# Kernel tuning notes

Measured on AMD Instinct MI355X. Metric: run time of the kernel, lower is better.

The kernel has to match this reference:

```python
import jax, jax.numpy as jnp
from jax import lax
import numpy as np

DIM = 256
QK = 256          # qk_dim defaults to dim
HEADS = 8
NWIN = 7
TOPK = 4
KS = 3            # side_dwconv


def setup_inputs() -> dict:
    key = jax.random.key(0)
    ks = jax.random.split(key, 8)
    B, H, W = 1, 112, 112
    s = lambda d: 1.0 / np.sqrt(d)
    return {
        "x": jax.random.normal(ks[0], (B, H, W, DIM), jnp.float32),
        # fused qkv linear: dim -> qk + qk + dim
        "w_qkv": jax.random.normal(ks[1], (DIM, 2 * QK + DIM), jnp.float32) * s(DIM),
        "b_qkv": jnp.zeros((2 * QK + DIM,), jnp.float32),
        # output projection
        "w_o": jax.random.normal(ks[2], (DIM, DIM), jnp.float32) * s(DIM),
        "b_o": jnp.zeros((DIM,), jnp.float32),
        # depthwise 3x3 lepe conv (HWIO with I=1, groups=dim)
        "lepe_w": jax.random.normal(ks[3], (KS, KS, 1, DIM), jnp.float32) * s(KS * KS),
        "lepe_b": jnp.zeros((DIM,), jnp.float32),
    }


def _win2img(t, B, H, W, c):
    # (B, p2, h, w, c) windows -> (B, H, W, c) image
    hw, ww = H // NWIN, W // NWIN
    t = t.reshape(B, NWIN, NWIN, hw, ww, c)
    return t.transpose(0, 1, 3, 2, 4, 5).reshape(B, H, W, c)


def reference(x, w_qkv, b_qkv, w_o, b_o, lepe_w, lepe_b):
    B, H, W, C = x.shape
    hw, ww = H // NWIN, W // NWIN
    p2, w2 = NWIN * NWIN, hw * ww
    hd_q, hd_v = QK // HEADS, DIM // HEADS
    scale = QK ** (-0.5)

    # partition into windows: (B, p2, hw, ww, C)
    xp = x.reshape(B, NWIN, hw, NWIN, ww, C).transpose(0, 1, 3, 2, 4, 5)
    xp = xp.reshape(B, p2, hw, ww, C)

    qkv = xp @ w_qkv + b_qkv
    q, kv = qkv[..., :QK], qkv[..., QK:]          # (B,p2,hw,ww,QK), (...,QK+DIM)

    q_pix = q.reshape(B, p2, w2, QK)
    kv_pix = kv.reshape(B, p2, w2, QK + DIM)      # identity kv_down

    # region-level routing (detached in original since diff_routing=False)
    q_win = lax.stop_gradient(q.mean((2, 3)))     # (B,p2,QK)
    k_win = lax.stop_gradient(kv[..., :QK].mean((2, 3)))
    logit = (q_win * scale) @ jnp.swapaxes(k_win, -1, -2)   # (B,p2,p2)
    top_logit, top_idx = lax.top_k(logit, TOPK)             # (B,p2,TOPK)
    r_weight = jax.nn.softmax(top_logit, axis=-1)           # unused: mul_weight='none'

    # gather top-k regions' KV: (B, p2, TOPK, w2, QK+DIM)
    kv_sel = jax.vmap(lambda kvb, idxb: kvb[idxb])(kv_pix, top_idx)

    k_sel = kv_sel[..., :QK].reshape(B, p2, TOPK * w2, HEADS, hd_q)
    v_sel = kv_sel[..., QK:].reshape(B, p2, TOPK * w2, HEADS, hd_v)
    qh = q_pix.reshape(B, p2, w2, HEADS, hd_q)

    attn = jnp.einsum('bpqhc,bpkhc->bphqk', qh * scale, k_sel)
    attn = jax.nn.softmax(attn, axis=-1)
    out = jnp.einsum('bphqk,bpkhc->bpqhc', attn, v_sel).reshape(B, p2, hw, ww, DIM)
    out = _win2img(out, B, H, W, DIM)

    # lepe: depthwise conv over v in image layout
    v_img = _win2img(kv[..., QK:], B, H, W, DIM)
    lepe = lax.conv_general_dilated(
        v_img, lepe_w, (1, 1), 'SAME',
        dimension_numbers=('NHWC', 'HWIO', 'NHWC'),
        feature_group_count=DIM) + lepe_b

    return (out + lepe) @ w_o + b_o
```

## Files before the change

### kernel.cpp

```cpp
#include <hip/hip_runtime.h>
#include <math.h>


typedef __bf16 bf16x8 __attribute__((ext_vector_type(8)));
typedef __bf16 bf16x4 __attribute__((ext_vector_type(4)));
typedef float f32x4 __attribute__((ext_vector_type(4)));

__global__ __launch_bounds__(64)
void pack1(const float* __restrict__ x, const float* __restrict__ w_qkv,
           const float* __restrict__ w_o, __bf16* __restrict__ xbf,
           __bf16* __restrict__ wtq, __bf16* __restrict__ wto) {
    const int b = blockIdx.x;
    const int t = threadIdx.x;
    if (b < 12544) {
        int p = b >> 8, pix = b & 255;
        int hh = (p / 7) * 16 + (pix >> 4);
        int ww = (p % 7) * 16 + (pix & 15);
        const float* src = x + ((size_t)(hh * 112 + ww)) * 256 + t * 4;
        float4 v = *(const float4*)src;
        bf16x4 o;
        o[0] = (__bf16)v.x; o[1] = (__bf16)v.y; o[2] = (__bf16)v.z; o[3] = (__bf16)v.w;
        *(bf16x4*)(xbf + (size_t)b * 256 + t * 4) = o;
    } else if (b < 12544 + 768) {
        int n = b - 12544;
        int k = t * 4;
        bf16x4 o;
        o[0] = (__bf16)w_qkv[(k + 0) * 768 + n];
        o[1] = (__bf16)w_qkv[(k + 1) * 768 + n];
        o[2] = (__bf16)w_qkv[(k + 2) * 768 + n];
        o[3] = (__bf16)w_qkv[(k + 3) * 768 + n];
        *(bf16x4*)(wtq + (size_t)n * 256 + k) = o;
    } else {
        int n = b - 12544 - 768;
        int k = t * 4;
        bf16x4 o;
        o[0] = (__bf16)w_o[(k + 0) * 256 + n];
        o[1] = (__bf16)w_o[(k + 1) * 256 + n];
        o[2] = (__bf16)w_o[(k + 2) * 256 + n];
        o[3] = (__bf16)w_o[(k + 3) * 256 + n];
        *(bf16x4*)(wto + (size_t)n * 256 + k) = o;
    }
}

template<int QKV>
__global__ __launch_bounds__(256)
void gemm_bf16(const __bf16* __restrict__ A,
               const __bf16* __restrict__ Wt,
               const float* __restrict__ bias,
               float* __restrict__ C, int N,
               __bf16* __restrict__ Qp,
               __bf16* __restrict__ Kp,
               __bf16* __restrict__ vbf,
               __bf16* __restrict__ Vt) {
    const int t = threadIdx.x & 63;
    const int wv = threadIdx.x >> 6;
    const int l16 = t & 15, quad = t >> 4;
    const int m0 = blockIdx.x * 64;
    const int n0 = blockIdx.y * 128 + wv * 32;

    __shared__ __bf16 Vs[128][72];

    f32x4 acc[2][4];
#pragma unroll
    for (int km = 0; km < 2; km++)
#pragma unroll
        for (int nt = 0; nt < 4; nt++) acc[km][nt] = (f32x4){0.f, 0.f, 0.f, 0.f};

#pragma unroll
    for (int ks = 0; ks < 8; ks++) {
        bf16x8 Af[2], Bf[4];
#pragma unroll
        for (int km = 0; km < 2; km++)
            Af[km] = *(const bf16x8*)(Wt + (size_t)(n0 + km * 16 + l16) * 256 + ks * 32 + quad * 8);
#pragma unroll
        for (int nt = 0; nt < 4; nt++)
            Bf[nt] = *(const bf16x8*)(A + (size_t)(m0 + nt * 16 + l16) * 256 + ks * 32 + quad * 8);
#pragma unroll
        for (int km = 0; km < 2; km++)
#pragma unroll
            for (int nt = 0; nt < 4; nt++)
                acc[km][nt] = __builtin_amdgcn_mfma_f32_16x16x32_bf16(
                    Af[km], Bf[nt], acc[km][nt], 0, 0, 0);
    }

#pragma unroll
    for (int km = 0; km < 2; km++) {
        const int n = n0 + km * 16 + quad * 4;
        float4 b4 = *(const float4*)(bias + n);
#pragma unroll
        for (int nt = 0; nt < 4; nt++) {
            const int m = m0 + nt * 16 + l16;
            float v0 = acc[km][nt][0] + b4.x;
            float v1 = acc[km][nt][1] + b4.y;
            float v2 = acc[km][nt][2] + b4.z;
            float v3 = acc[km][nt][3] + b4.w;
            if (QKV == 0) {
                float4 o = {v0, v1, v2, v3};
                *(float4*)(C + (size_t)m * N + n) = o;
            } else {
                const int p = m >> 8, pix = m & 255;
                if (n0 < 256) {
                    const float s = 1.0f / 16.0f;
                    int h = n >> 5, cc = n & 31;
                    bf16x4 o;
                    o[0] = (__bf16)(v0 * s); o[1] = (__bf16)(v1 * s);
                    o[2] = (__bf16)(v2 * s); o[3] = (__bf16)(v3 * s);
                    *(bf16x4*)(Qp + ((size_t)((p * 8 + h) * 256 + pix)) * 32 + cc) = o;
                } else if (n0 < 512) {
                    int n2 = n - 256;
                    int h = n2 >> 5, cc = n2 & 31;
                    bf16x4 o;
                    o[0] = (__bf16)v0; o[1] = (__bf16)v1;
                    o[2] = (__bf16)v2; o[3] = (__bf16)v3;
                    *(bf16x4*)(Kp + ((size_t)((p * 8 + h) * 256 + pix)) * 32 + cc) = o;
                } else {
                    int n2 = n - 512;
                    int imgrow = ((p / 7) * 16 + (pix >> 4)) * 112 + (p % 7) * 16 + (pix & 15);
                    bf16x4 o;
                    o[0] = (__bf16)v0; o[1] = (__bf16)v1;
                    o[2] = (__bf16)v2; o[3] = (__bf16)v3;
                    *(bf16x4*)(vbf + (size_t)imgrow * 256 + n2) = o;
                    const int cbase = wv * 32 + km * 16 + quad * 4;
                    const int pb = nt * 16 + l16;
                    Vs[cbase + 0][pb] = o[0];
                    Vs[cbase + 1][pb] = o[1];
                    Vs[cbase + 2][pb] = o[2];
                    Vs[cbase + 3][pb] = o[3];
                }
            }
        }
    }

    if (QKV == 1 && blockIdx.y >= 4) {
        __syncthreads();
        const int p_ = m0 >> 8, qt_ = (m0 >> 6) & 3;
        const int vb = blockIdx.y * 128 - 512;
#pragma unroll
        for (int rep = 0; rep < 4; rep++) {
            int id = rep * 256 + threadIdx.x;
            int row = id >> 3, c8 = (id & 7) * 8;
            int hh = (vb + row) >> 5, c32 = (vb + row) & 31;
            bf16x8 val = *(const bf16x8*)&Vs[row][c8];
            *(bf16x8*)(Vt + ((size_t)((p_ * 8 + hh) * 32 + c32)) * 256 + qt_ * 64 + c8) = val;
        }
    }
}

__global__ __launch_bounds__(256)
void win_means(const __bf16* __restrict__ Qp,
               const __bf16* __restrict__ Kp,
               float* __restrict__ q_win, float* __restrict__ k_win) {
    const int b = blockIdx.x;
    const int p = b >> 3, h = b & 7;
    const int t = threadIdx.x;
    const int c8 = (t & 3) * 8;
    const int r0 = t >> 2;
    float aq[8], ak[8];
#pragma unroll
    for (int j = 0; j < 8; j++) { aq[j] = 0.f; ak[j] = 0.f; }
#pragma unroll
    for (int rg = 0; rg < 4; rg++) {
        const int r = rg * 64 + r0;
        bf16x8 q = *(const bf16x8*)(Qp + ((size_t)(b * 256 + r)) * 32 + c8);
        bf16x8 k = *(const bf16x8*)(Kp + ((size_t)(b * 256 + r)) * 32 + c8);
#pragma unroll
        for (int j = 0; j < 8; j++) { aq[j] += (float)q[j]; ak[j] += (float)k[j]; }
    }
    __shared__ float Sq[256][8], Sk[256][8];
#pragma unroll
    for (int j = 0; j < 8; j++) { Sq[t][j] = aq[j]; Sk[t][j] = ak[j]; }
    __syncthreads();
    if (t < 32) {
        const int grp = t >> 3, cj = t & 7;
        float sq = 0.f, sk = 0.f;
        for (int i = 0; i < 64; i++) {
            sq += Sq[i * 4 + grp][cj];
            sk += Sk[i * 4 + grp][cj];
        }
        q_win[p * 256 + h * 32 + t] = sq * (1.f / 256.f);
        k_win[p * 256 + h * 32 + t] = sk * (1.f / 256.f);
    }
}

__global__ __launch_bounds__(64)
void routing_topk(const float* __restrict__ q_win,
                  const float* __restrict__ k_win,
                  int* __restrict__ top_idx) {
    const int r = blockIdx.x;
    const int j = threadIdx.x;
    __shared__ float vals[64];

    float d = -1e30f;
    if (j < 49) {
        const float4* qp = (const float4*)(q_win + r * 256);
        const float4* kp = (const float4*)(k_win + j * 256);
        float s = 0.f;
#pragma unroll
        for (int c = 0; c < 64; c++) {
            float4 a = qp[c], b = kp[c];
            s += a.x * b.x + a.y * b.y + a.z * b.z + a.w * b.w;
        }
        d = s;
    }
    vals[j] = d;
    __syncthreads();
    if (j == 0) {
        float bv0 = -1e30f, bv1 = -1e30f, bv2 = -1e30f, bv3 = -1e30f;
        int bi0 = 0, bi1 = 0, bi2 = 0, bi3 = 0;
        for (int q = 0; q < 49; q++) {
            float v = vals[q];
            if (v > bv0) {
                bv3 = bv2; bi3 = bi2; bv2 = bv1; bi2 = bi1; bv1 = bv0; bi1 = bi0;
                bv0 = v; bi0 = q;
            } else if (v > bv1) {
                bv3 = bv2; bi3 = bi2; bv2 = bv1; bi2 = bi1; bv1 = v; bi1 = q;
            } else if (v > bv2) {
                bv3 = bv2; bi3 = bi2; bv2 = v; bi2 = q;
            } else if (v > bv3) {
                bv3 = v; bi3 = q;
            }
        }
        top_idx[r * 4 + 0] = bi0;
        top_idx[r * 4 + 1] = bi1;
        top_idx[r * 4 + 2] = bi2;
        top_idx[r * 4 + 3] = bi3;
    }
}

#define PLDS_PITCH 68
#define HALO_PITCH 36

__global__ __launch_bounds__(64)
void attn_mfma(const __bf16* __restrict__ Qp,
               const __bf16* __restrict__ Kp,
               const __bf16* __restrict__ Vt,
               const int* __restrict__ top_idx,
               const __bf16* __restrict__ vbf,
               const float* __restrict__ lw,
               const float* __restrict__ lb,
               __bf16* __restrict__ prebf) {
    const int bb = blockIdx.x;
    const int qt = bb / 392;
    const int ph = bb - qt * 392;
    const int p = ph >> 3;
    const int h = ph & 7;
    const int t = threadIdx.x;
    const int l16 = t & 15, quad = t >> 4;

    __shared__ unsigned short Plds[64 * PLDS_PITCH];
    __shared__ __bf16 Hs[108 * HALO_PITCH];

    bf16x8 Qf[4];
#pragma unroll
    for (int nt = 0; nt < 4; nt++)
        Qf[nt] = *(const bf16x8*)(Qp + ((size_t)((p * 8 + h) * 256 + qt * 64 + nt * 16 + l16)) * 32 + quad * 8);

    float lstate[4] = {0.f, 0.f, 0.f, 0.f};
    f32x4 O[2][4];
#pragma unroll
    for (int mt = 0; mt < 2; mt++)
#pragma unroll
        for (int nt = 0; nt < 4; nt++) O[mt][nt] = (f32x4){0.f, 0.f, 0.f, 0.f};

    int sels[4];
#pragma unroll
    for (int s = 0; s < 4; s++) sels[s] = top_idx[p * 4 + s];

    bf16x8 Kf[4];
    {
        const __bf16* Kb = Kp + ((size_t)(sels[0] * 8 + h)) * 8192;
#pragma unroll
        for (int km = 0; km < 4; km++)
            Kf[km] = *(const bf16x8*)(Kb + (size_t)(km * 16 + l16) * 32 + quad * 8);
    }

    for (int kc = 0; kc < 16; kc++) {
        const int sel = sels[kc >> 2];
        const int kbase = (kc & 3) * 64;

        const __bf16* Vb = Vt + ((size_t)(sel * 8 + h)) * 8192;
        bf16x8 Vf[2][2];
#pragma unroll
        for (int kstep = 0; kstep < 2; kstep++)
#pragma unroll
            for (int mt = 0; mt < 2; mt++)
                Vf[kstep][mt] = *(const bf16x8*)(Vb + (size_t)(mt * 16 + l16) * 256 + kbase + kstep * 32 + quad * 8);

        const int kcn = (kc < 15) ? kc + 1 : 15;
        const __bf16* Kbn = Kp + ((size_t)(sels[kcn >> 2] * 8 + h)) * 8192;
        const int kbn = (kcn & 3) * 64;
        bf16x8 Kn[4];
#pragma unroll
        for (int km = 0; km < 4; km++)
            Kn[km] = *(const bf16x8*)(Kbn + (size_t)(kbn + km * 16 + l16) * 32 + quad * 8);

#pragma unroll
        for (int nt = 0; nt < 4; nt++) {
            f32x4 S[4];
#pragma unroll
            for (int km = 0; km < 4; km++)
                S[km] = __builtin_amdgcn_mfma_f32_16x16x32_bf16(
                    Kf[km], Qf[nt], (f32x4){0.f, 0.f, 0.f, 0.f}, 0, 0, 0);

            float rs = 0.f;
#pragma unroll
            for (int km = 0; km < 4; km++) {
                union { unsigned short u[4]; ushort4 v; } pk;
#pragma unroll
                for (int r = 0; r < 4; r++) {
                    float pv = __expf(S[km][r]);
                    rs += pv;
                    pk.u[r] = __builtin_bit_cast(unsigned short, (__bf16)pv);
                }
                *(ushort4*)&Plds[(nt * 16 + l16) * PLDS_PITCH + km * 16 + quad * 4] = pk.v;
            }
            rs += __shfl_xor(rs, 16);
            rs += __shfl_xor(rs, 32);
            lstate[nt] += rs;
        }

#pragma unroll
        for (int kstep = 0; kstep < 2; kstep++) {
#pragma unroll
            for (int nt = 0; nt < 4; nt++) {
                int idx = (nt * 16 + l16) * PLDS_PITCH + kstep * 32 + quad * 8;
                union { ushort4 u4[2]; bf16x8 v; } pu;
                pu.u4[0] = *(const ushort4*)&Plds[idx];
                pu.u4[1] = *(const ushort4*)&Plds[idx + 4];
#pragma unroll
                for (int mt = 0; mt < 2; mt++)
                    O[mt][nt] = __builtin_amdgcn_mfma_f32_16x16x32_bf16(
                        Vf[kstep][mt], pu.v, O[mt][nt], 0, 0, 0);
            }
        }

#pragma unroll
        for (int km = 0; km < 4; km++) Kf[km] = Kn[km];
    }

    const int pr = p / 7, pc = p % 7;
    for (int i = t; i < 108; i += 64) {
        int hy = i / 18, hx = i - hy * 18;
        int gy = pr * 16 + qt * 4 - 1 + hy;
        int gx = pc * 16 - 1 + hx;
        union { bf16x4 v4[8]; bf16x8 v8[4]; uint4 q[4]; } u;
        u.q[0] = (uint4){0u, 0u, 0u, 0u};
        u.q[1] = (uint4){0u, 0u, 0u, 0u};
        u.q[2] = (uint4){0u, 0u, 0u, 0u};
        u.q[3] = (uint4){0u, 0u, 0u, 0u};
        if (gy >= 0 && gy < 112 && gx >= 0 && gx < 112) {
            const __bf16* src = vbf + ((size_t)(gy * 112 + gx)) * 256 + h * 32;
            u.v8[0] = *(const bf16x8*)src;
            u.v8[1] = *(const bf16x8*)(src + 8);
            u.v8[2] = *(const bf16x8*)(src + 16);
            u.v8[3] = *(const bf16x8*)(src + 24);
        }
#pragma unroll
        for (int j = 0; j < 8; j++)
            *(bf16x4*)&Hs[i * HALO_PITCH + j * 4] = u.v4[j];
    }
    __syncthreads();

#pragma unroll
    for (int mt = 0; mt < 2; mt++) {
        const int c = h * 32 + mt * 16 + quad * 4;
        const float4 lbv = *(const float4*)(lb + c);
        float a0[4], a1[4], a2[4], a3[4];
#pragma unroll
        for (int nt = 0; nt < 4; nt++) {
            a0[nt] = lbv.x; a1[nt] = lbv.y; a2[nt] = lbv.z; a3[nt] = lbv.w;
        }
#pragma unroll
        for (int dh = 0; dh < 3; dh++)
#pragma unroll
            for (int dw = 0; dw < 3; dw++) {
                const float4 w4 = *(const float4*)(lw + (dh * 3 + dw) * 256 + c);
#pragma unroll
                for (int nt = 0; nt < 4; nt++) {
                    const bf16x4 v4 = *(const bf16x4*)&Hs[((nt + dh) * 18 + l16 + dw) * HALO_PITCH + mt * 16 + quad * 4];
                    a0[nt] += (float)v4[0] * w4.x;
                    a1[nt] += (float)v4[1] * w4.y;
                    a2[nt] += (float)v4[2] * w4.z;
                    a3[nt] += (float)v4[3] * w4.w;
                }
            }
#pragma unroll
        for (int nt = 0; nt < 4; nt++) {
            const float inv = 1.f / lstate[nt];
            bf16x4 ob;
            ob[0] = (__bf16)(O[mt][nt][0] * inv + a0[nt]);
            ob[1] = (__bf16)(O[mt][nt][1] * inv + a1[nt]);
            ob[2] = (__bf16)(O[mt][nt][2] * inv + a2[nt]);
            ob[3] = (__bf16)(O[mt][nt][3] * inv + a3[nt]);
            const int himg = pr * 16 + qt * 4 + nt, wimg = pc * 16 + l16;
            *(bf16x4*)(prebf + ((size_t)(himg * 112 + wimg)) * 256 + c) = ob;
        }
    }
}

extern "C" void kernel_launch(void* const* d_in, const int* in_sizes, int n_in,
                              void* d_out, int out_size, void* d_ws, size_t ws_size,
                              hipStream_t stream) {
    const float* x      = (const float*)d_in[0];
    const float* w_qkv  = (const float*)d_in[1];
    const float* b_qkv  = (const float*)d_in[2];
    const float* w_o    = (const float*)d_in[3];
    const float* b_o    = (const float*)d_in[4];
    const float* lepe_w = (const float*)d_in[5];
    const float* lepe_b = (const float*)d_in[6];
    float* out = (float*)d_out;

    char* w = (char*)d_ws;
    __bf16* Qp    = (__bf16*)w; w += 6422528;
    __bf16* Kp    = (__bf16*)w; w += 6422528;
    __bf16* vbf   = (__bf16*)w; w += 6422528;
    __bf16* Vt    = (__bf16*)w; w += 6422528;
    __bf16* xbf   = (__bf16*)w;
    __bf16* prebf = (__bf16*)w; w += 6422528;
    __bf16* wtq   = (__bf16*)w; w += 393216;
    __bf16* wto   = (__bf16*)w; w += 131072;
    float* q_win   = (float*)w; w += 12544 * 4;
    float* k_win   = (float*)w; w += 12544 * 4;
    int*   top_idx = (int*)w;

    pack1<<<12544 + 768 + 256, 64, 0, stream>>>(x, w_qkv, w_o, xbf, wtq, wto);
    gemm_bf16<1><<<dim3(196, 6), 256, 0, stream>>>(xbf, wtq, b_qkv,
                                                   nullptr, 0, Qp, Kp, vbf, Vt);
    win_means<<<392, 256, 0, stream>>>(Qp, Kp, q_win, k_win);
    routing_topk<<<49, 64, 0, stream>>>(q_win, k_win, top_idx);
    attn_mfma<<<392 * 4, 64, 0, stream>>>(Qp, Kp, Vt, top_idx,
                                          vbf, lepe_w, lepe_b, prebf);
    gemm_bf16<0><<<dim3(196, 2), 256, 0, stream>>>(prebf, wto, b_o,
                                                   out, 256, nullptr, nullptr, nullptr, nullptr);
}
```

Before: 192.2 us.

## Split attention KV regions across four waves with LDS reduction, use exp2

```diff
diff --git a/kernel.cpp b/kernel.cpp
--- a/kernel.cpp
+++ b/kernel.cpp
@@ -100,7 +100,7 @@
             } else {
                 const int p = m >> 8, pix = m & 255;
                 if (n0 < 256) {
-                    const float s = 1.0f / 16.0f;
+                    const float s = 1.4426950408889634f / 16.0f;
                     int h = n >> 5, cc = n & 31;
                     bf16x4 o;
                     o[0] = (__bf16)(v0 * s); o[1] = (__bf16)(v1 * s);
@@ -230,7 +230,7 @@
 #define PLDS_PITCH 68
 #define HALO_PITCH 36
 
-__global__ __launch_bounds__(64)
+__global__ __launch_bounds__(256)
 void attn_mfma(const __bf16* __restrict__ Qp,
                const __bf16* __restrict__ Kp,
                const __bf16* __restrict__ Vt,
@@ -244,17 +244,30 @@
     const int ph = bb - qt * 392;
     const int p = ph >> 3;
     const int h = ph & 7;
-    const int t = threadIdx.x;
+    const int t = threadIdx.x & 63;
+    const int wv = threadIdx.x >> 6;
     const int l16 = t & 15, quad = t >> 4;
 
-    __shared__ unsigned short Plds[64 * PLDS_PITCH];
+    __shared__ union {
+        unsigned short Plds[4][64 * PLDS_PITCH];
+        struct {
+            f32x4 O[4][2][4][64];
+            float l[4][4][64];
+        } red;
+    } U;
     __shared__ __bf16 Hs[108 * HALO_PITCH];
+
+    unsigned short* const Pw = U.Plds[wv];
 
     bf16x8 Qf[4];
 #pragma unroll
     for (int nt = 0; nt < 4; nt++)
         Qf[nt] = *(const bf16x8*)(Qp + ((size_t)((p * 8 + h) * 256 + qt * 64 + nt * 16 + l16)) * 32 + quad * 8);
 
+    const int sel = top_idx[p * 4 + wv];
+    const __bf16* const Kb = Kp + ((size_t)(sel * 8 + h)) * 8192;
+    const __bf16* const Vb = Vt + ((size_t)(sel * 8 + h)) * 8192;
+
     float lstate[4] = {0.f, 0.f, 0.f, 0.f};
     f32x4 O[2][4];
 #pragma unroll
@@ -262,37 +275,26 @@
 #pragma unroll
         for (int nt = 0; nt < 4; nt++) O[mt][nt] = (f32x4){0.f, 0.f, 0.f, 0.f};
 
-    int sels[4];
-#pragma unroll
-    for (int s = 0; s < 4; s++) sels[s] = top_idx[p * 4 + s];
-
     bf16x8 Kf[4];
-    {
-        const __bf16* Kb = Kp + ((size_t)(sels[0] * 8 + h)) * 8192;
+#pragma unroll
+    for (int km = 0; km < 4; km++)
+        Kf[km] = *(const bf16x8*)(Kb + (size_t)(km * 16 + l16) * 32 + quad * 8);
+
+    for (int kc = 0; kc < 4; kc++) {
+        const int kbase = kc * 64;
+
+        bf16x8 Vf[2][2];
+#pragma unroll
+        for (int ks = 0; ks < 2; ks++)
+#pragma unroll
+            for (int mt = 0; mt < 2; mt++)
+                Vf[ks][mt] = *(const bf16x8*)(Vb + (size_t)(mt * 16 + l16) * 256 + kbase + ks * 32 + quad * 8);
+
+        const int kbn = (kc < 3 ? kc + 1 : 3) * 64;
+        bf16x8 Kn[4];
 #pragma unroll
         for (int km = 0; km < 4; km++)
-            Kf[km] = *(const bf16x8*)(Kb + (size_t)(km * 16 + l16) * 32 + quad * 8);
-    }
-
-    for (int kc = 0; kc < 16; kc++) {
-        const int sel = sels[kc >> 2];
-        const int kbase = (kc & 3) * 64;
-
-        const __bf16* Vb = Vt + ((size_t)(sel * 8 + h)) * 8192;
-        bf16x8 Vf[2][2];
-#pragma unroll
-        for (int kstep = 0; kstep < 2; kstep++)
-#pragma unroll
-            for (int mt = 0; mt < 2; mt++)
-                Vf[kstep][mt] = *(const bf16x8*)(Vb + (size_t)(mt * 16 + l16) * 256 + kbase + kstep * 32 + quad * 8);
-
-        const int kcn = (kc < 15) ? kc + 1 : 15;
-        const __bf16* Kbn = Kp + ((size_t)(sels[kcn >> 2] * 8 + h)) * 8192;
-        const int kbn = (kcn & 3) * 64;
-        bf16x8 Kn[4];
-#pragma unroll
-        for (int km = 0; km < 4; km++)
-            Kn[km] = *(const bf16x8*)(Kbn + (size_t)(kbn + km * 16 + l16) * 32 + quad * 8);
+            Kn[km] = *(const bf16x8*)(Kb + (size_t)(kbn + km * 16 + l16) * 32 + quad * 8);
 
 #pragma unroll
         for (int nt = 0; nt < 4; nt++) {
@@ -308,11 +310,11 @@
                 union { unsigned short u[4]; ushort4 v; } pk;
 #pragma unroll
                 for (int r = 0; r < 4; r++) {
-                    float pv = __expf(S[km][r]);
+                    float pv = __builtin_amdgcn_exp2f(S[km][r]);
                     rs += pv;
                     pk.u[r] = __builtin_bit_cast(unsigned short, (__bf16)pv);
                 }
-                *(ushort4*)&Plds[(nt * 16 + l16) * PLDS_PITCH + km * 16 + quad * 4] = pk.v;
+                *(ushort4*)&Pw[(nt * 16 + l16) * PLDS_PITCH + km * 16 + quad * 4] = pk.v;
             }
             rs += __shfl_xor(rs, 16);
             rs += __shfl_xor(rs, 32);
@@ -320,17 +322,17 @@
         }
 
 #pragma unroll
-        for (int kstep = 0; kstep < 2; kstep++) {
+        for (int ks = 0; ks < 2; ks++) {
 #pragma unroll
             for (int nt = 0; nt < 4; nt++) {
-                int idx = (nt * 16 + l16) * PLDS_PITCH + kstep * 32 + quad * 8;
+                int idx = (nt * 16 + l16) * PLDS_PITCH + ks * 32 + quad * 8;
                 union { ushort4 u4[2]; bf16x8 v; } pu;
-                pu.u4[0] = *(const ushort4*)&Plds[idx];
-                pu.u4[1] = *(const ushort4*)&Plds[idx + 4];
+                pu.u4[0] = *(const ushort4*)&Pw[idx];
+                pu.u4[1] = *(const ushort4*)&Pw[idx + 4];
 #pragma unroll
                 for (int mt = 0; mt < 2; mt++)
                     O[mt][nt] = __builtin_amdgcn_mfma_f32_16x16x32_bf16(
-                        Vf[kstep][mt], pu.v, O[mt][nt], 0, 0, 0);
+                        Vf[ks][mt], pu.v, O[mt][nt], 0, 0, 0);
             }
         }
 
@@ -338,8 +340,19 @@
         for (int km = 0; km < 4; km++) Kf[km] = Kn[km];
     }
 
+    __syncthreads();
+#pragma unroll
+    for (int mt = 0; mt < 2; mt++)
+#pragma unroll
+        for (int nt = 0; nt < 4; nt++)
+            U.red.O[wv][mt][nt][t] = O[mt][nt];
+#pragma unroll
+    for (int nt = 0; nt < 4; nt++)
+        U.red.l[wv][nt][t] = lstate[nt];
+
     const int pr = p / 7, pc = p % 7;
-    for (int i = t; i < 108; i += 64) {
+    if (threadIdx.x < 108) {
+        const int i = threadIdx.x;
         int hy = i / 18, hx = i - hy * 18;
         int gy = pr * 16 + qt * 4 - 1 + hy;
         int gx = pc * 16 - 1 + hx;
@@ -361,40 +374,39 @@
     }
     __syncthreads();
 
+    const int nt = wv;
+    const float ltot = U.red.l[0][nt][t] + U.red.l[1][nt][t]
+                     + U.red.l[2][nt][t] + U.red.l[3][nt][t];
+    const float inv = 1.f / ltot;
+    const int himg = pr * 16 + qt * 4 + nt, wimg = pc * 16 + l16;
 #pragma unroll
     for (int mt = 0; mt < 2; mt++) {
+        f32x4 o = U.red.O[0][mt][nt][t];
+#pragma unroll
+        for (int v = 1; v < 4; v++) {
+            f32x4 ov = U.red.O[v][mt][nt][t];
+            o[0] += ov[0]; o[1] += ov[1]; o[2] += ov[2]; o[3] += ov[3];
+        }
         const int c = h * 32 + mt * 16 + quad * 4;
         const float4 lbv = *(const float4*)(lb + c);
-        float a0[4], a1[4], a2[4], a3[4];
-#pragma unroll
-        for (int nt = 0; nt < 4; nt++) {
-            a0[nt] = lbv.x; a1[nt] = lbv.y; a2[nt] = lbv.z; a3[nt] = lbv.w;
-        }
+        float a0 = lbv.x, a1 = lbv.y, a2 = lbv.z, a3 = lbv.w;
 #pragma unroll
         for (int dh = 0; dh < 3; dh++)
 #pragma unroll
             for (int dw = 0; dw < 3; dw++) {
                 const float4 w4 = *(const float4*)(lw + (dh * 3 + dw) * 256 + c);
-#pragma unroll
-                for (int nt = 0; nt < 4; nt++) {
-                    const bf16x4 v4 = *(const bf16x4*)&Hs[((nt + dh) * 18 + l16 + dw) * HALO_PITCH + mt * 16 + quad * 4];
-                    a0[nt] += (float)v4[0] * w4.x;
-                    a1[nt] += (float)v4[1] * w4.y;
-                    a2[nt] += (float)v4[2] * w4.z;
-                    a3[nt] += (float)v4[3] * w4.w;
-                }
+                const bf16x4 v4 = *(const bf16x4*)&Hs[((nt + dh) * 18 + l16 + dw) * HALO_PITCH + mt * 16 + quad * 4];
+                a0 += (float)v4[0] * w4.x;
+                a1 += (float)v4[1] * w4.y;
+                a2 += (float)v4[2] * w4.z;
+                a3 += (float)v4[3] * w4.w;
             }
-#pragma unroll
-        for (int nt = 0; nt < 4; nt++) {
-            const float inv = 1.f / lstate[nt];
-            bf16x4 ob;
-            ob[0] = (__bf16)(O[mt][nt][0] * inv + a0[nt]);
-            ob[1] = (__bf16)(O[mt][nt][1] * inv + a1[nt]);
-            ob[2] = (__bf16)(O[mt][nt][2] * inv + a2[nt]);
-            ob[3] = (__bf16)(O[mt][nt][3] * inv + a3[nt]);
-            const int himg = pr * 16 + qt * 4 + nt, wimg = pc * 16 + l16;
-            *(bf16x4*)(prebf + ((size_t)(himg * 112 + wimg)) * 256 + c) = ob;
-        }
+        bf16x4 ob;
+        ob[0] = (__bf16)(o[0] * inv + a0);
+        ob[1] = (__bf16)(o[1] * inv + a1);
+        ob[2] = (__bf16)(o[2] * inv + a2);
+        ob[3] = (__bf16)(o[3] * inv + a3);
+        *(bf16x4*)(prebf + ((size_t)(himg * 112 + wimg)) * 256 + c) = ob;
     }
 }
 
@@ -428,8 +440,8 @@
                                                    nullptr, 0, Qp, Kp, vbf, Vt);
     win_means<<<392, 256, 0, stream>>>(Qp, Kp, q_win, k_win);
     routing_topk<<<49, 64, 0, stream>>>(q_win, k_win, top_idx);
-    attn_mfma<<<392 * 4, 64, 0, stream>>>(Qp, Kp, Vt, top_idx,
-                                          vbf, lepe_w, lepe_b, prebf);
+    attn_mfma<<<392 * 4, 256, 0, stream>>>(Qp, Kp, Vt, top_idx,
+                                           vbf, lepe_w, lepe_b, prebf);
     gemm_bf16<0><<<dim3(196, 2), 256, 0, stream>>>(prebf, wto, b_o,
                                                    out, 256, nullptr, nullptr, nullptr, nullptr);
 }
```

New measurement: 183.0 us. 1.05x faster.
